# Kernel tuning notes

Hardware: AMD Instinct MI355X
Metric: run time of the kernel (lower is better)

Reference implementation:

```python
import jax, jax.numpy as jnp
import numpy as np

N_NEWS = 200000
N_COMPANIES = 10000
N_EDGES = 640000
HIDDEN = 256


def setup_inputs() -> dict:
    key = jax.random.key(0)
    ks = jax.random.split(key, 7)
    scale = 1.0 / np.sqrt(HIDDEN)  # keep tanh out of full saturation
    news_x = jax.random.normal(ks[0], (N_NEWS, HIDDEN), dtype=jnp.float32)
    company_x = jax.random.normal(ks[1], (N_COMPANIES, HIDDEN), dtype=jnp.float32)
    W_news = jax.random.normal(ks[2], (HIDDEN, HIDDEN), dtype=jnp.float32) * scale
    W_company = jax.random.normal(ks[3], (HIDDEN, HIDDEN), dtype=jnp.float32) * scale
    v = jax.random.normal(ks[4], (HIDDEN,), dtype=jnp.float32) * scale
    src = jax.random.randint(ks[5], (N_EDGES,), 0, N_NEWS, dtype=jnp.int64)
    dst = jax.random.randint(ks[6], (N_EDGES,), 0, N_COMPANIES, dtype=jnp.int64)
    return {
        "news_x": news_x,
        "company_x": company_x,
        "W_news": W_news,
        "W_company": W_company,
        "v": v,
        "src": src,
        "dst": dst,
        "num_companies": N_COMPANIES,
    }


def reference(news_x, company_x, W_news, W_company, v, src, dst, num_companies):
    # Gather per-edge endpoint features, project (nn.Linear applies x @ W.T).
    news_part = news_x[src] @ W_news.T          # [E, H]
    company_part = company_x[dst] @ W_company.T  # [E, H]
    scores = jnp.tanh(news_part + company_part) @ v  # [E]

    # Segment-wise (per-company) numerically stable softmax over incoming edges.
    smax = jax.ops.segment_max(scores, dst, num_segments=num_companies)  # [C]
    scores_exp = jnp.exp(scores - smax[dst])                             # [E]
    denom = jax.ops.segment_sum(scores_exp, dst, num_segments=num_companies)[dst]
    weights = scores_exp / jnp.clip(denom, 1e-9)                         # [E]

    # Weighted scatter-add of raw news features into company slots.
    out = jax.ops.segment_sum(news_x[src] * weights[:, None], dst,
                              num_segments=num_companies)               # [C, H]
    return out
```

## Files before the change

### kernel.cpp

```cpp
#include <hip/hip_runtime.h>
#include <hip/hip_bf16.h>
#include <cmath>
#include <cstdint>


#define H 256

typedef __attribute__((ext_vector_type(8))) short bfrag;
typedef __attribute__((ext_vector_type(4))) float ffrag;

__device__ __forceinline__ ushort f2bf(float f) {
  uint u = __float_as_uint(f);
  uint r = u + 0x7FFFu + ((u >> 16) & 1u);
  return (ushort)(r >> 16);
}
__device__ __forceinline__ float bf2f(ushort h) {
  return __uint_as_float((uint)h << 16);
}

__global__ void prep_kernel(const float* __restrict__ Wn, const float* __restrict__ Wc,
                            ushort* __restrict__ WnHi, ushort* __restrict__ WnLo,
                            ushort* __restrict__ WcHi, ushort* __restrict__ WcLo,
                            const int* __restrict__ dst, int* __restrict__ counts, int E) {
  const int b = blockIdx.x, tid = threadIdx.x;
  if (b < 256) {
    int i = b * 256 + tid;
    float w = Wn[i];
    ushort h = f2bf(w);
    WnHi[i] = h;
    WnLo[i] = f2bf(w - bf2f(h));
  } else if (b < 512) {
    int i = (b - 256) * 256 + tid;
    float w = Wc[i];
    ushort h = f2bf(w);
    WcHi[i] = h;
    WcLo[i] = f2bf(w - bf2f(h));
  } else {
    int e = (b - 512) * 256 + tid;
    if (e < E) atomicAdd(&counts[dst[e]], 1);
  }
}

__global__ void scan_kernel(const int* __restrict__ counts, int* __restrict__ offsets,
                            int* __restrict__ cursor, int C) {
  __shared__ int wsum[16];
  int tid = threadIdx.x;
  int lane = tid & 63, wid = tid >> 6;
  int base = 0;
  for (int start = 0; start < C; start += 1024) {
    int idx = start + tid;
    int val = (idx < C) ? counts[idx] : 0;
    int x = val;
#pragma unroll
    for (int off = 1; off < 64; off <<= 1) {
      int y = __shfl_up(x, off);
      if (lane >= off) x += y;
    }
    if (lane == 63) wsum[wid] = x;
    __syncthreads();
    int add = base;
    for (int w = 0; w < wid; ++w) add += wsum[w];
    if (idx < C) {
      int excl = add + x - val;
      offsets[idx] = excl;
      cursor[idx]  = excl;
    }
    int tot = 0;
#pragma unroll
    for (int w = 0; w < 16; ++w) tot += wsum[w];
    __syncthreads();
    base += tot;
  }
  if (tid == 0) offsets[C] = base;
}

__global__ void fill_kernel(const int* __restrict__ src, const int* __restrict__ dst,
                            int* __restrict__ cursor, int* __restrict__ srcs_sorted, int E) {
  int e = blockIdx.x * blockDim.x + threadIdx.x;
  if (e < E) {
    int d = dst[e];
    int pos = atomicAdd(&cursor[d], 1);
    srcs_sorted[pos] = src[e];
  }
}

__global__ __launch_bounds__(512, 2) void gemm_persist(
    const float* __restrict__ Xc, const ushort* __restrict__ WcHi,
    const ushort* __restrict__ WcLo, ushort* __restrict__ cproj, int MC, int GC,
    const float* __restrict__ Xn, const ushort* __restrict__ WnHi,
    const ushort* __restrict__ WnLo, ushort* __restrict__ nproj,
    ushort* __restrict__ nxbf, int MN) {
  constexpr int PITCH = 264;
  __shared__ ushort Xs[2][64 * PITCH];
  const int tid = threadIdx.x;
  const int wv = tid >> 6, lane = tid & 63;
  const int q = lane >> 4, nidx = lane & 15;
  const int GN = gridDim.x - GC;

  const float* X; const ushort *Whi, *Wlo; ushort *proj, *xb; int M, nb, lb;
  if ((int)blockIdx.x < GC) {
    X = Xc; Whi = WcHi; Wlo = WcLo; proj = cproj; xb = nullptr; M = MC;
    nb = GC; lb = blockIdx.x;
  } else {
    X = Xn; Whi = WnHi; Wlo = WnLo; proj = nproj; xb = nxbf; M = MN;
    nb = GN; lb = blockIdx.x - GC;
  }
  const int nt = (M + 63) >> 6;
  const int qt = nt / nb, rt = nt % nb;
  const int first = lb * qt + (lb < rt ? lb : rt);
  const int cnt = qt + (lb < rt ? 1 : 0);
  if (cnt <= 0) return;

  bfrag bhi[8][2], blo[8][2];
#pragma unroll
  for (int ks = 0; ks < 8; ++ks)
#pragma unroll
    for (int tt = 0; tt < 2; ++tt) {
      const size_t off = (size_t)(wv * 32 + tt * 16 + nidx) * H + ks * 32 + q * 8;
      bhi[ks][tt] = *(const bfrag*)(Whi + off);
      blo[ks][tt] = *(const bfrag*)(Wlo + off);
    }

  float4 xr[8];
  auto load8 = [&](int tile) {
#pragma unroll
    for (int j = 0; j < 8; ++j) {
      const int flat = j * 2048 + tid * 4;
      int gr = tile * 64 + (flat >> 8);
      if (gr >= M) gr = M - 1;
      xr[j] = *(const float4*)(X + (size_t)gr * H + (flat & 255));
    }
  };
  auto writebuf = [&](int p, int tile) {
#pragma unroll
    for (int j = 0; j < 8; ++j) {
      const int flat = j * 2048 + tid * 4;
      const int r = flat >> 8, k = flat & 255;
      ushort4 b4;
      b4.x = f2bf(xr[j].x); b4.y = f2bf(xr[j].y);
      b4.z = f2bf(xr[j].z); b4.w = f2bf(xr[j].w);
      *(ushort4*)&Xs[p][r * PITCH + k] = b4;
      if (xb) {
        const int gr = tile * 64 + r;
        *(ushort4*)(xb + (size_t)gr * H + k) = b4;
      }
    }
  };

  load8(first);
  writebuf(0, first);
  if (cnt > 1) load8(first + 1);
  int p = 0;
  for (int t = 0; t < cnt; ++t) {
    __syncthreads();
    const int tile = first + t;

    ffrag acc[4][2];
#pragma unroll
    for (int i = 0; i < 4; ++i) { acc[i][0] = (ffrag)(0.f); acc[i][1] = (ffrag)(0.f); }
#pragma unroll
    for (int ks = 0; ks < 8; ++ks) {
      bfrag a[4];
#pragma unroll
      for (int i = 0; i < 4; ++i)
        a[i] = *(const bfrag*)&Xs[p][(16 * i + nidx) * PITCH + ks * 32 + q * 8];
#pragma unroll
      for (int i = 0; i < 4; ++i)
#pragma unroll
        for (int tt = 0; tt < 2; ++tt) {
          acc[i][tt] = __builtin_amdgcn_mfma_f32_16x16x32_bf16(a[i], bhi[ks][tt], acc[i][tt], 0, 0, 0);
          acc[i][tt] = __builtin_amdgcn_mfma_f32_16x16x32_bf16(a[i], blo[ks][tt], acc[i][tt], 0, 0, 0);
        }
    }

    const int row0 = tile * 64;
#pragma unroll
    for (int i = 0; i < 4; ++i)
#pragma unroll
      for (int r = 0; r < 4; ++r) {
        const int grow = row0 + 16 * i + q * 4 + r;
        if (grow < M) {
#pragma unroll
          for (int tt = 0; tt < 2; ++tt)
            proj[(size_t)grow * H + wv * 32 + tt * 16 + nidx] = f2bf(acc[i][tt][r]);
        }
      }

    if (t + 1 < cnt) writebuf(p ^ 1, tile + 1);
    if (t + 2 < cnt) load8(tile + 2);
    p ^= 1;
  }
}

__device__ __forceinline__ float fast_tanh(float x) {
  float e = __builtin_amdgcn_exp2f(x * 2.8853900817779268f);
  float t = __builtin_amdgcn_rcpf(e + 1.f);
  return __builtin_fmaf(-2.f, t, 1.f);
}

__global__ __launch_bounds__(256) void edge_flash_kernel(
    const ushort* __restrict__ news_projbf, const ushort* __restrict__ company_projbf,
    const float* __restrict__ v, const int* __restrict__ offsets,
    const int* __restrict__ srcs, const ushort* __restrict__ news_xbf,
    float* __restrict__ out) {
  const int c = blockIdx.x;
  const int tid = threadIdx.x;
  const int sl = tid & 31;
  const int hw = tid >> 5;
  __shared__ float cp[H];
  __shared__ float mW[8], lW[8];
  __shared__ float OW[8][H];
  cp[tid] = bf2f(company_projbf[(size_t)c * H + tid]);
  __syncthreads();
  const float4 va = *(const float4*)(v + sl * 8);
  const float4 vb = *(const float4*)(v + sl * 8 + 4);
  const float4 ca = *(const float4*)&cp[sl * 8];
  const float4 cb = *(const float4*)&cp[sl * 8 + 4];
  const float vv[8] = {va.x, va.y, va.z, va.w, vb.x, vb.y, vb.z, vb.w};
  const float cq[8] = {ca.x, ca.y, ca.z, ca.w, cb.x, cb.y, cb.z, cb.w};
  const int beg = offsets[c], end = offsets[c + 1];

  float m = -INFINITY, l = 0.f;
  float O[8] = {0.f, 0.f, 0.f, 0.f, 0.f, 0.f, 0.f, 0.f};

  int i = beg + hw;
  if (i < end) {
    int s = srcs[i];
    bfrag pr = *(const bfrag*)(news_projbf + (size_t)s * H + sl * 8);
    bfrag xr = *(const bfrag*)(news_xbf + (size_t)s * H + sl * 8);
    for (;;) {
      const int inext = i + 8;
      const bool more = (inext < end);
      bfrag prn, xrn;
      if (more) {
        int sn = srcs[inext];
        prn = *(const bfrag*)(news_projbf + (size_t)sn * H + sl * 8);
        xrn = *(const bfrag*)(news_xbf + (size_t)sn * H + sl * 8);
      }
      float r = 0.f;
#pragma unroll
      for (int j = 0; j < 8; ++j)
        r += fast_tanh(bf2f((ushort)pr[j]) + cq[j]) * vv[j];
#pragma unroll
      for (int off = 16; off > 0; off >>= 1) r += __shfl_xor(r, off);
      const float mnew = fmaxf(m, r);
      const float alpha = __expf(m - mnew);
      const float pa = __expf(r - mnew);
      l = l * alpha + pa;
#pragma unroll
      for (int j = 0; j < 8; ++j)
        O[j] = O[j] * alpha + pa * bf2f((ushort)xr[j]);
      m = mnew;
      i = inext;
      if (!more) break;
      pr = prn; xr = xrn;
    }
  }

  if (sl == 0) { mW[hw] = m; lW[hw] = l; }
  *(float4*)&OW[hw][sl * 8]     = make_float4(O[0], O[1], O[2], O[3]);
  *(float4*)&OW[hw][sl * 8 + 4] = make_float4(O[4], O[5], O[6], O[7]);
  __syncthreads();
  float mstar = -INFINITY;
#pragma unroll
  for (int w = 0; w < 8; ++w) mstar = fmaxf(mstar, mW[w]);
  float denom = 0.f, val = 0.f;
#pragma unroll
  for (int w = 0; w < 8; ++w) {
    const float sc = (lW[w] > 0.f) ? __expf(mW[w] - mstar) : 0.f;
    denom += lW[w] * sc;
    val += OW[w][tid] * sc;
  }
  out[(size_t)c * H + tid] = val / fmaxf(denom, 1e-9f);
}

extern "C" void kernel_launch(void* const* d_in, const int* in_sizes, int n_in,
                              void* d_out, int out_size, void* d_ws, size_t ws_size,
                              hipStream_t stream) {
  const float* news_x    = (const float*)d_in[0];
  const float* company_x = (const float*)d_in[1];
  const float* W_news    = (const float*)d_in[2];
  const float* W_company = (const float*)d_in[3];
  const float* v         = (const float*)d_in[4];
  const int*   src       = (const int*)d_in[5];
  const int*   dst       = (const int*)d_in[6];
  const int N = in_sizes[0] / H;
  const int C = in_sizes[1] / H;
  const int E = in_sizes[5];
  float* out = (float*)d_out;

  char* p = (char*)d_ws;
  ushort* news_projbf    = (ushort*)p; p += (size_t)N * H * sizeof(ushort);
  ushort* news_xbf       = (ushort*)p; p += (size_t)N * H * sizeof(ushort);
  ushort* company_projbf = (ushort*)p; p += (size_t)C * H * sizeof(ushort);
  int*    srcs_sorted    = (int*)p;    p += (size_t)E * sizeof(int);
  ushort* Wn_hi          = (ushort*)p; p += (size_t)H * H * sizeof(ushort);
  ushort* Wn_lo          = (ushort*)p; p += (size_t)H * H * sizeof(ushort);
  ushort* Wc_hi          = (ushort*)p; p += (size_t)H * H * sizeof(ushort);
  ushort* Wc_lo          = (ushort*)p; p += (size_t)H * H * sizeof(ushort);
  int*    counts         = (int*)p;    p += (size_t)C * sizeof(int);
  int*    offsets        = (int*)p;    p += (size_t)(C + 1) * sizeof(int);
  int*    cursor         = (int*)p;    p += (size_t)C * sizeof(int);

  hipMemsetAsync(counts, 0, (size_t)C * sizeof(int), stream);
  prep_kernel<<<512 + (E + 255) / 256, 256, 0, stream>>>(
      W_news, W_company, Wn_hi, Wn_lo, Wc_hi, Wc_lo, dst, counts, E);
  scan_kernel<<<1, 1024, 0, stream>>>(counts, offsets, cursor, C);
  fill_kernel<<<(E + 255) / 256, 256, 0, stream>>>(src, dst, cursor, srcs_sorted, E);

  const int GC = 12, GN = 244;
  gemm_persist<<<GC + GN, 512, 0, stream>>>(
      company_x, Wc_hi, Wc_lo, company_projbf, C, GC,
      news_x, Wn_hi, Wn_lo, news_projbf, news_xbf, N);

  edge_flash_kernel<<<C, 256, 0, stream>>>(news_projbf, company_projbf, v, offsets,
                                           srcs_sorted, news_xbf, out);
}
```

Before: 533.4 us.

## Widen GEMM blocks to 1024 threads with one output tile per wave

```diff
diff --git a/kernel.cpp b/kernel.cpp
--- a/kernel.cpp
+++ b/kernel.cpp
@@ -84,7 +84,7 @@
   }
 }
 
-__global__ __launch_bounds__(512, 2) void gemm_persist(
+__global__ __launch_bounds__(1024, 1) void gemm_persist(
     const float* __restrict__ Xc, const ushort* __restrict__ WcHi,
     const ushort* __restrict__ WcLo, ushort* __restrict__ cproj, int MC, int GC,
     const float* __restrict__ Xn, const ushort* __restrict__ WnHi,
@@ -111,21 +111,19 @@
   const int cnt = qt + (lb < rt ? 1 : 0);
   if (cnt <= 0) return;
 
-  bfrag bhi[8][2], blo[8][2];
-#pragma unroll
-  for (int ks = 0; ks < 8; ++ks)
-#pragma unroll
-    for (int tt = 0; tt < 2; ++tt) {
-      const size_t off = (size_t)(wv * 32 + tt * 16 + nidx) * H + ks * 32 + q * 8;
-      bhi[ks][tt] = *(const bfrag*)(Whi + off);
-      blo[ks][tt] = *(const bfrag*)(Wlo + off);
-    }
-
-  float4 xr[8];
-  auto load8 = [&](int tile) {
-#pragma unroll
-    for (int j = 0; j < 8; ++j) {
-      const int flat = j * 2048 + tid * 4;
+  bfrag bhi[8], blo[8];
+#pragma unroll
+  for (int ks = 0; ks < 8; ++ks) {
+    const size_t off = (size_t)(wv * 16 + nidx) * H + ks * 32 + q * 8;
+    bhi[ks] = *(const bfrag*)(Whi + off);
+    blo[ks] = *(const bfrag*)(Wlo + off);
+  }
+
+  float4 xr[4];
+  auto load4 = [&](int tile) {
+#pragma unroll
+    for (int j = 0; j < 4; ++j) {
+      const int flat = j * 4096 + tid * 4;
       int gr = tile * 64 + (flat >> 8);
       if (gr >= M) gr = M - 1;
       xr[j] = *(const float4*)(X + (size_t)gr * H + (flat & 255));
@@ -133,8 +131,8 @@
   };
   auto writebuf = [&](int p, int tile) {
 #pragma unroll
-    for (int j = 0; j < 8; ++j) {
-      const int flat = j * 2048 + tid * 4;
+    for (int j = 0; j < 4; ++j) {
+      const int flat = j * 4096 + tid * 4;
       const int r = flat >> 8, k = flat & 255;
       ushort4 b4;
       b4.x = f2bf(xr[j].x); b4.y = f2bf(xr[j].y);
@@ -147,17 +145,18 @@
     }
   };
 
-  load8(first);
+  load4(first);
   writebuf(0, first);
-  if (cnt > 1) load8(first + 1);
   int p = 0;
   for (int t = 0; t < cnt; ++t) {
     __syncthreads();
     const int tile = first + t;
-
-    ffrag acc[4][2];
-#pragma unroll
-    for (int i = 0; i < 4; ++i) { acc[i][0] = (ffrag)(0.f); acc[i][1] = (ffrag)(0.f); }
+    const bool more = (t + 1 < cnt);
+    if (more) load4(tile + 1);
+
+    ffrag acc[4];
+#pragma unroll
+    for (int i = 0; i < 4; ++i) acc[i] = (ffrag)(0.f);
 #pragma unroll
     for (int ks = 0; ks < 8; ++ks) {
       bfrag a[4];
@@ -165,12 +164,10 @@
       for (int i = 0; i < 4; ++i)
         a[i] = *(const bfrag*)&Xs[p][(16 * i + nidx) * PITCH + ks * 32 + q * 8];
 #pragma unroll
-      for (int i = 0; i < 4; ++i)
-#pragma unroll
-        for (int tt = 0; tt < 2; ++tt) {
-          acc[i][tt] = __builtin_amdgcn_mfma_f32_16x16x32_bf16(a[i], bhi[ks][tt], acc[i][tt], 0, 0, 0);
-          acc[i][tt] = __builtin_amdgcn_mfma_f32_16x16x32_bf16(a[i], blo[ks][tt], acc[i][tt], 0, 0, 0);
-        }
+      for (int i = 0; i < 4; ++i) {
+        acc[i] = __builtin_amdgcn_mfma_f32_16x16x32_bf16(a[i], bhi[ks], acc[i], 0, 0, 0);
+        acc[i] = __builtin_amdgcn_mfma_f32_16x16x32_bf16(a[i], blo[ks], acc[i], 0, 0, 0);
+      }
     }
 
     const int row0 = tile * 64;
@@ -179,15 +176,11 @@
 #pragma unroll
       for (int r = 0; r < 4; ++r) {
         const int grow = row0 + 16 * i + q * 4 + r;
-        if (grow < M) {
-#pragma unroll
-          for (int tt = 0; tt < 2; ++tt)
-            proj[(size_t)grow * H + wv * 32 + tt * 16 + nidx] = f2bf(acc[i][tt][r]);
-        }
+        if (grow < M)
+          proj[(size_t)grow * H + wv * 16 + nidx] = f2bf(acc[i][r]);
       }
 
-    if (t + 1 < cnt) writebuf(p ^ 1, tile + 1);
-    if (t + 2 < cnt) load8(tile + 2);
+    if (more) writebuf(p ^ 1, tile + 1);
     p ^= 1;
   }
 }
@@ -309,7 +302,7 @@
   fill_kernel<<<(E + 255) / 256, 256, 0, stream>>>(src, dst, cursor, srcs_sorted, E);
 
   const int GC = 12, GN = 244;
-  gemm_persist<<<GC + GN, 512, 0, stream>>>(
+  gemm_persist<<<GC + GN, 1024, 0, stream>>>(
       company_x, Wc_hi, Wc_lo, company_projbf, C, GC,
       news_x, Wn_hi, Wn_lo, news_projbf, news_xbf, N);
 
```

Measured after the change: 533.4 us. No clear change (-0.0%).
